# Optimization experiments

Hardware: AMD Instinct MI355X
Metric: run time of the kernel (lower is better)

The kernel has to match this reference:

```python
import jax, jax.numpy as jnp
from jax import lax
import numpy as np

RANK = 128
INPUT_DIM = 128
OUT_DIM = 32
N = 128
L = 512
INIT_STD = 1.0 / np.sqrt(RANK * INPUT_DIM)  # variance-preserving recurrence


def setup_inputs() -> dict:
    key = jax.random.key(0)
    k_x, k_A, k_a, k_O = jax.random.split(key, 4)
    x = jax.random.normal(k_x, (N, L, INPUT_DIM), dtype=jnp.float32)
    A = INIT_STD * jax.random.normal(k_A, (RANK, INPUT_DIM, RANK), dtype=jnp.float32)
    alpha = INIT_STD * jax.random.normal(k_a, (RANK,), dtype=jnp.float32)
    Omega = INIT_STD * jax.random.normal(k_O, (RANK, OUT_DIM), dtype=jnp.float32)
    return {"x": x, "alpha": alpha, "A": A, "Omega": Omega}


def reference(x, alpha, A, Omega):
    # x: [N, L, D]; alpha: [R]; A: [R, D, R]; Omega: [R, M]
    # h_0 = einsum('i,ijk,nj->nk', alpha, A, x[:,0])
    h0 = jnp.einsum('i,ijk,nj->nk', alpha, A, x[:, 0, :])

    def step(h, xt):
        # h: [N, R], xt: [N, D] -> new h: [N, R]
        h = jnp.einsum('ni,ijk,nj->nk', h, A, xt)
        return h, None

    xs = jnp.swapaxes(x, 0, 1)[1:]  # [L-1, N, D]
    h, _ = lax.scan(step, h0, xs)
    out = jnp.einsum('ni,im->nm', h, Omega)  # [N, M]
    return jnp.squeeze(out)
```

## Files before the change

### kernel.cpp

```cpp
#include <hip/hip_runtime.h>

typedef _Float16 f16;
typedef _Float16 half8 __attribute__((ext_vector_type(8)));
typedef _Float16 half4v __attribute__((ext_vector_type(4)));
typedef float f32x4 __attribute__((ext_vector_type(4)));


__global__ void k_cvt_x(const float* __restrict__ in, f16* __restrict__ out) {
    int idx = blockIdx.x * blockDim.x + threadIdx.x;
    float4 v = ((const float4*)in)[idx];
    half4v o;
    o[0] = (f16)v.x; o[1] = (f16)v.y; o[2] = (f16)v.z; o[3] = (f16)v.w;
    ((half4v*)out)[idx] = o;
}

__global__ void k_cvt_A(const float* __restrict__ A, f16* __restrict__ Af2) {
    int o = blockIdx.x * blockDim.x + threadIdx.x;
    int i = o >> 14;
    int k = (o >> 7) & 127;
    int j = o & 127;
    Af2[o] = (f16)A[(i << 14) + (j << 7) + k];
}

__device__ __forceinline__
void gemm_body(f16* lA, f16* lX, const f16* __restrict__ Af2, const f16* __restrict__ Xh,
               f16* __restrict__ B, int t0, int logTc, int qtile, int i, int tid) {
    const int row = tid >> 4;
    const int ch = tid & 15;
    const int Tcm1 = (1 << logTc) - 1;

    {
        const f16* srcA = Af2 + ((size_t)i << 14);
#pragma unroll
        for (int r = 0; r < 128; r += 16) {
            int rr = row + r;
            uint4 v = *(const uint4*)(srcA + (rr << 7) + (ch << 3));
            *(uint4*)(&lA[(rr << 7) + ((ch ^ (rr & 15)) << 3)]) = v;
        }
#pragma unroll
        for (int r = 0; r < 128; r += 16) {
            int rr = row + r;
            int qr = (qtile << 7) + rr;
            int n = qr >> logTc;
            int trel = qr & Tcm1;
            const f16* srcX = Xh + (((size_t)(n << 9) + t0 + trel) << 7);
            uint4 v = *(const uint4*)(srcX + (ch << 3));
            *(uint4*)(&lX[(rr << 7) + ((ch ^ (rr & 15)) << 3)]) = v;
        }
    }
    __syncthreads();

    const int wave = tid >> 6;
    const int lane = tid & 63;
    const int l15 = lane & 15;
    const int l4 = lane >> 4;
    f32x4 acc[8][2] = {};

#pragma unroll
    for (int ks = 0; ks < 4; ++ks) {
        const int c = (ks << 2) + l4;
        half8 afr[8], bfr[2];
#pragma unroll
        for (int mt = 0; mt < 8; ++mt) {
            int rowA = (mt << 4) + l15;
            afr[mt] = *(const half8*)(&lA[(rowA << 7) + ((c ^ l15) << 3)]);
        }
#pragma unroll
        for (int qt = 0; qt < 2; ++qt) {
            int rowX = (wave << 5) + (qt << 4) + l15;
            bfr[qt] = *(const half8*)(&lX[(rowX << 7) + ((c ^ l15) << 3)]);
        }
#pragma unroll
        for (int mt = 0; mt < 8; ++mt)
#pragma unroll
            for (int qt = 0; qt < 2; ++qt)
                acc[mt][qt] = __builtin_amdgcn_mfma_f32_16x16x32_f16(
                    afr[mt], bfr[qt], acc[mt][qt], 0, 0, 0);
    }

    __syncthreads();
    f16* stage = lA;
#pragma unroll
    for (int mt = 0; mt < 8; ++mt)
#pragma unroll
        for (int qt = 0; qt < 2; ++qt) {
            int q = (wave << 5) + (qt << 4) + l15;
            int chunk = (mt << 1) + (l4 >> 1);
            int hf = l4 & 1;
            half4v o;
            o[0] = (f16)acc[mt][qt][0];
            o[1] = (f16)acc[mt][qt][1];
            o[2] = (f16)acc[mt][qt][2];
            o[3] = (f16)acc[mt][qt][3];
            *(half4v*)(&stage[(q << 7) + (((chunk ^ l15) << 3) + (hf << 2))]) = o;
        }
    __syncthreads();
    {
        const int lr = lane >> 4;
        const int lc = lane & 15;
#pragma unroll
        for (int it = 0; it < 8; ++it) {
            int q = (wave << 5) + (it << 2) + lr;
            uint4 v = *(const uint4*)(&stage[(q << 7) + ((lc ^ (q & 15)) << 3)]);
            size_t qg = (size_t)((qtile << 7) + q);
            *(uint4*)(B + (qg << 14) + (i << 7) + (lc << 3)) = v;
        }
    }
}

__device__ __forceinline__
void chain_body(float* hl, float (*part)[132], const f16* __restrict__ B,
                float* __restrict__ hstate, const float* __restrict__ alpha,
                const float* __restrict__ Om, float* __restrict__ out,
                int Tc, int first, int last, int n, int tid) {
    const int kg = tid & 15;
    const int iq = tid >> 4;

    if (tid < 128) hl[tid] = first ? alpha[tid] : hstate[(n << 7) + tid];
    __syncthreads();

    const f16* bbase = B + (((size_t)n * Tc) << 14) + (iq << 10) + (kg << 3);
    half8 buf[4][8];
#pragma unroll
    for (int s = 0; s < 4; ++s)
#pragma unroll
        for (int ii = 0; ii < 8; ++ii)
            buf[s][ii] = *(const half8*)(bbase + ((size_t)s << 14) + (ii << 7));

    for (int t = 0; t < Tc; t += 4) {
#pragma unroll
        for (int s = 0; s < 4; ++s) {
            float4 h0 = *(const float4*)&hl[iq << 3];
            float4 h1 = *(const float4*)&hl[(iq << 3) + 4];
            float acc[8] = {0, 0, 0, 0, 0, 0, 0, 0};
#pragma unroll
            for (int ii = 0; ii < 4; ++ii) {
                float hv = (&h0.x)[ii];
#pragma unroll
                for (int j = 0; j < 8; ++j)
                    acc[j] += hv * (float)buf[s][ii][j];
            }
#pragma unroll
            for (int ii = 0; ii < 4; ++ii) {
                float hv = (&h1.x)[ii];
#pragma unroll
                for (int j = 0; j < 8; ++j)
                    acc[j] += hv * (float)buf[s][ii + 4][j];
            }
            int tn = t + s + 4;
            if (tn < Tc) {
#pragma unroll
                for (int ii = 0; ii < 8; ++ii)
                    buf[s][ii] = *(const half8*)(bbase + ((size_t)tn << 14) + (ii << 7));
            }
            *(float4*)(&part[iq][kg << 3])       = make_float4(acc[0], acc[1], acc[2], acc[3]);
            *(float4*)(&part[iq][(kg << 3) + 4]) = make_float4(acc[4], acc[5], acc[6], acc[7]);
            __syncthreads();
            if (tid < 128) {
                float s0 = part[0][tid] + part[1][tid];
                float s1 = part[2][tid] + part[3][tid];
                float s2 = part[4][tid] + part[5][tid];
                float s3 = part[6][tid] + part[7][tid];
                s0 += part[8][tid] + part[9][tid];
                s1 += part[10][tid] + part[11][tid];
                s2 += part[12][tid] + part[13][tid];
                s3 += part[14][tid] + part[15][tid];
                hl[tid] = (s0 + s1) + (s2 + s3);
            }
            __syncthreads();
        }
    }

    if (!last) {
        if (tid < 128) hstate[(n << 7) + tid] = hl[tid];
    } else if (tid < 32) {
        float s = 0.f;
        for (int i2 = 0; i2 < 128; ++i2) s += hl[i2] * Om[(i2 << 5) + tid];
        out[(n << 5) + tid] = s;
    }
}

__global__ __launch_bounds__(256, 2)
void k_gemm(const f16* __restrict__ Af2, const f16* __restrict__ Xh,
            f16* __restrict__ B, int t0, int logTc) {
    __shared__ __align__(16) char smem[65536];
    gemm_body((f16*)smem, (f16*)(smem + 32768), Af2, Xh, B, t0, logTc,
              blockIdx.x, blockIdx.y, threadIdx.x);
}

__global__ __launch_bounds__(256, 2)
void k_chain(const f16* __restrict__ B, float* __restrict__ hstate,
             const float* __restrict__ alpha, const float* __restrict__ Om,
             float* __restrict__ out, int Tc, int first, int last) {
    __shared__ __align__(16) char smem[16384];
    chain_body((float*)smem, (float(*)[132])(smem + 512), B, hstate, alpha, Om, out,
               Tc, first, last, blockIdx.x, threadIdx.x);
}

__global__ __launch_bounds__(256, 2)
void k_fused(const f16* __restrict__ Af2, const f16* __restrict__ Xh,
             f16* __restrict__ Bw, const f16* __restrict__ Br,
             float* __restrict__ hstate, const float* __restrict__ alpha,
             const float* __restrict__ Om, float* __restrict__ out,
             int t0g, int logTc, int Tc, int first, int last) {
    __shared__ __align__(16) char smem[65536];
    const int bx = blockIdx.x;
    if (bx < 128) {
        chain_body((float*)smem, (float(*)[132])(smem + 512), Br, hstate, alpha, Om, out,
                   Tc, first, last, bx, threadIdx.x);
    } else {
        int g = bx - 128;
        int qtile = g & (Tc - 1);
        int i = g >> logTc;
        gemm_body((f16*)smem, (f16*)(smem + 32768), Af2, Xh, Bw, t0g, logTc,
                  qtile, i, threadIdx.x);
    }
}

extern "C" void kernel_launch(void* const* d_in, const int* in_sizes, int n_in,
                              void* d_out, int out_size, void* d_ws, size_t ws_size,
                              hipStream_t stream) {
    const float* x     = (const float*)d_in[0];
    const float* alpha = (const float*)d_in[1];
    const float* A     = (const float*)d_in[2];
    const float* Om    = (const float*)d_in[3];
    float* out = (float*)d_out;

    char* ws = (char*)d_ws;
    f16*   Af2    = (f16*)ws;
    f16*   Xh     = (f16*)(ws + ((size_t)4 << 20));
    float* hstate = (float*)(ws + ((size_t)20 << 20));

    int Tc = 16;
    while (Tc > 4 && ((size_t)21 << 20) + (((size_t)Tc << 22) * 2) > ws_size) Tc >>= 1;
    int logTc = 31 - __builtin_clz(Tc);
    int nch = 512 / Tc;
    f16* Bc[2];
    Bc[0] = (f16*)(ws + ((size_t)21 << 20));
    Bc[1] = (f16*)(ws + ((size_t)21 << 20) + ((size_t)Tc << 22));

    k_cvt_x<<<8192, 256, 0, stream>>>(x, Xh);
    k_cvt_A<<<8192, 256, 0, stream>>>(A, Af2);

    k_gemm<<<dim3(Tc, 128), 256, 0, stream>>>(Af2, Xh, Bc[0], 0, logTc);

    for (int c = 0; c < nch; ++c) {
        const f16* br = Bc[c & 1];
        if (c + 1 < nch) {
            k_fused<<<128 + Tc * 128, 256, 0, stream>>>(
                Af2, Xh, Bc[(c + 1) & 1], br, hstate, alpha, Om, out,
                (c + 1) * Tc, logTc, Tc, c == 0, c == nch - 1);
        } else {
            k_chain<<<128, 256, 0, stream>>>(br, hstate, alpha, Om, out,
                                             Tc, c == 0, c == nch - 1);
        }
    }
    (void)in_sizes; (void)n_in; (void)out_size;
}
```

Before: 970.2 us.

## Merge conversion kernels and overlap x conversion with first GEMM chunk

Only the first 16 timesteps of x, the ones the first GEMM chunk needs, are now converted in a combined pre-kernel alongside the A transpose. The rest of x is converted by extra blocks inside the first GEMM launch, so that work overlaps the GEMM. This removes a launch and takes most of the x conversion off the critical path. A block-index permutation for the chain blocks is also added, probably to spread them across XCDs or CUs, and the offset-based indexing adds complexity.

```diff
diff --git a/kernel.cpp b/kernel.cpp
--- a/kernel.cpp
+++ b/kernel.cpp
@@ -6,20 +6,22 @@
 typedef float f32x4 __attribute__((ext_vector_type(4)));
 
 
-__global__ void k_cvt_x(const float* __restrict__ in, f16* __restrict__ out) {
-    int idx = blockIdx.x * blockDim.x + threadIdx.x;
-    float4 v = ((const float4*)in)[idx];
-    half4v o;
-    o[0] = (f16)v.x; o[1] = (f16)v.y; o[2] = (f16)v.z; o[3] = (f16)v.w;
-    ((half4v*)out)[idx] = o;
-}
-
-__global__ void k_cvt_A(const float* __restrict__ A, f16* __restrict__ Af2) {
-    int o = blockIdx.x * blockDim.x + threadIdx.x;
-    int i = o >> 14;
-    int k = (o >> 7) & 127;
-    int j = o & 127;
-    Af2[o] = (f16)A[(i << 14) + (j << 7) + k];
+__global__ void k_cvt_pre(const float* __restrict__ x, f16* __restrict__ Xh,
+                          const float* __restrict__ A, f16* __restrict__ Af2) {
+    int b = blockIdx.x;
+    if (b < 256) {
+        int tid = (b << 8) + threadIdx.x;
+        int n = tid >> 9;
+        int rem = tid & 511;
+        int off = (n << 16) + (rem << 2);
+        float4 v = *(const float4*)(x + off);
+        half4v o; o[0] = (f16)v.x; o[1] = (f16)v.y; o[2] = (f16)v.z; o[3] = (f16)v.w;
+        *(half4v*)(Xh + off) = o;
+    } else {
+        int o = ((b - 256) << 8) + threadIdx.x;
+        int i = o >> 14, k = (o >> 7) & 127, j = o & 127;
+        Af2[o] = (f16)A[(i << 14) + (j << 7) + k];
+    }
 }
 
 __device__ __forceinline__
@@ -180,21 +182,38 @@
     }
 }
 
+__device__ __forceinline__ int chain_n(int bx, int logTc) {
+    if (logTc == 4) return (bx & 64) | ((bx & 7) << 3) | ((bx >> 3) & 7);
+    return bx;
+}
+
 __global__ __launch_bounds__(256, 2)
-void k_gemm(const f16* __restrict__ Af2, const f16* __restrict__ Xh,
-            f16* __restrict__ B, int t0, int logTc) {
+void k_gemm0(const f16* __restrict__ Af2, const f16* __restrict__ Xh,
+             f16* __restrict__ B, const float* __restrict__ x, int logTc) {
     __shared__ __align__(16) char smem[65536];
-    gemm_body((f16*)smem, (f16*)(smem + 32768), Af2, Xh, B, t0, logTc,
-              blockIdx.x, blockIdx.y, threadIdx.x);
+    const int bx = blockIdx.x;
+    const int Tc = 1 << logTc;
+    const int ngemm = Tc << 7;
+    if (bx < ngemm) {
+        gemm_body((f16*)smem, (f16*)(smem + 32768), Af2, Xh, B, 0, logTc,
+                  bx & (Tc - 1), bx >> logTc, threadIdx.x);
+    } else {
+        int f = ((bx - ngemm) << 8) + threadIdx.x;
+        int t = (f & 16383) >> 5;
+        if (t < 16) return;
+        float4 v = *(const float4*)(x + ((size_t)f << 2));
+        half4v o; o[0] = (f16)v.x; o[1] = (f16)v.y; o[2] = (f16)v.z; o[3] = (f16)v.w;
+        *(half4v*)(Xh + ((size_t)f << 2)) = o;
+    }
 }
 
 __global__ __launch_bounds__(256, 2)
 void k_chain(const f16* __restrict__ B, float* __restrict__ hstate,
              const float* __restrict__ alpha, const float* __restrict__ Om,
-             float* __restrict__ out, int Tc, int first, int last) {
+             float* __restrict__ out, int Tc, int logTc, int first, int last) {
     __shared__ __align__(16) char smem[16384];
     chain_body((float*)smem, (float(*)[132])(smem + 512), B, hstate, alpha, Om, out,
-               Tc, first, last, blockIdx.x, threadIdx.x);
+               Tc, first, last, chain_n(blockIdx.x, logTc), threadIdx.x);
 }
 
 __global__ __launch_bounds__(256, 2)
@@ -207,7 +226,7 @@
     const int bx = blockIdx.x;
     if (bx < 128) {
         chain_body((float*)smem, (float(*)[132])(smem + 512), Br, hstate, alpha, Om, out,
-                   Tc, first, last, bx, threadIdx.x);
+                   Tc, first, last, chain_n(bx, logTc), threadIdx.x);
     } else {
         int g = bx - 128;
         int qtile = g & (Tc - 1);
@@ -239,10 +258,8 @@
     Bc[0] = (f16*)(ws + ((size_t)21 << 20));
     Bc[1] = (f16*)(ws + ((size_t)21 << 20) + ((size_t)Tc << 22));
 
-    k_cvt_x<<<8192, 256, 0, stream>>>(x, Xh);
-    k_cvt_A<<<8192, 256, 0, stream>>>(A, Af2);
-
-    k_gemm<<<dim3(Tc, 128), 256, 0, stream>>>(Af2, Xh, Bc[0], 0, logTc);
+    k_cvt_pre<<<256 + 8192, 256, 0, stream>>>(x, Xh, A, Af2);
+    k_gemm0<<<(Tc << 7) + 8192, 256, 0, stream>>>(Af2, Xh, Bc[0], x, logTc);
 
     for (int c = 0; c < nch; ++c) {
         const f16* br = Bc[c & 1];
@@ -252,7 +269,7 @@
                 (c + 1) * Tc, logTc, Tc, c == 0, c == nch - 1);
         } else {
             k_chain<<<128, 256, 0, stream>>>(br, hstate, alpha, Om, out,
-                                             Tc, c == 0, c == nch - 1);
+                                             Tc, logTc, c == 0, c == nch - 1);
         }
     }
     (void)in_sizes; (void)n_in; (void)out_size;
```

After: 961.3 us. No clear change (-0.9%).
